# Kernel optimization log

Measured on AMD Instinct MI355X. Metric: run time of the kernel, lower is better.

## Reference

```python
import jax, jax.numpy as jnp
import numpy as np

NUM_HEADS = 12
HEAD_SIZE = 64  # hidden_size // num_heads


def setup_inputs() -> dict:
    key = jax.random.key(0)
    ks = jax.random.split(key, 4)
    B, S, H = 2, 2048, 768
    return {
        "hidden_states": jax.random.normal(ks[0], (B, S, H), dtype=jnp.float32),
        "attention_mask": jnp.ones((B, S), dtype=jnp.int32),
        "Wq": jax.random.normal(ks[1], (H, H), dtype=jnp.float32) * 0.02,
        "bq": jnp.zeros((H,), dtype=jnp.float32),
        "Wk": jax.random.normal(ks[2], (H, H), dtype=jnp.float32) * 0.02,
        "bk": jnp.zeros((H,), dtype=jnp.float32),
        "Wv": jax.random.normal(ks[3], (H, H), dtype=jnp.float32) * 0.02,
        "bv": jnp.zeros((H,), dtype=jnp.float32),
    }


def reference(hidden_states, attention_mask, Wq, bq, Wk, bk, Wv, bv):
    B, S, H = hidden_states.shape
    nh, hs = NUM_HEADS, HEAD_SIZE

    def to_heads(x):  # [B,S,H] -> [nh,B,S,hs] (matches to_multi_head)
        return x.reshape(B, S, nh, hs).transpose(2, 0, 1, 3)

    # torch Linear: y = x @ W.T + b
    q = to_heads(hidden_states @ Wq.T + bq)
    k = to_heads(hidden_states @ Wk.T + bk)
    v = to_heads(hidden_states @ Wv.T + bv)

    scores = jnp.einsum("hbqd,hbkd->hbqk", q, k) / jnp.float32(hs) ** 0.5
    # mask: 1 -> attend, 0 -> -inf; broadcast over query dim
    m = 1.0 - attention_mask.astype(scores.dtype)
    add = jnp.where(m != 0.0, -jnp.inf, 0.0)[None, :, None, :]  # [1,B,1,S]
    probs = jax.nn.softmax(scores + add, axis=-1)
    # dropout is identity in eval mode
    out = jnp.einsum("hbqk,hbkd->hbqd", probs, v)
    # from_multi_head: [nh,B,S,hs] -> [B,S,H]
    return out.transpose(1, 2, 0, 3).reshape(B, S, H)
```

## Files before the change

### kernel.cpp

```cpp
#include <hip/hip_runtime.h>
#include <hip/hip_bf16.h>

#define BATCH 2
#define SEQ   2048
#define HID   768
#define NH    12
#define HS    64
#define MROWS (BATCH*SEQ)
#define N3    (3*HID)
#define HB    (NH*BATCH)

typedef __attribute__((ext_vector_type(8))) short short8;
typedef __attribute__((ext_vector_type(4))) short short4v;
typedef __attribute__((ext_vector_type(4))) float floatx4;

#ifndef __has_builtin
#define __has_builtin(x) 0
#endif
#if __has_builtin(__builtin_amdgcn_mfma_f32_16x16x16bf16_1k)
#define HAVE_K16 1
#else
#define HAVE_K16 0
#endif

#define QSCALE 0.1803368801111204f

__device__ __forceinline__ unsigned short f2bf(float x){
  __hip_bfloat16 h = __float2bfloat16(x);
  return __builtin_bit_cast(unsigned short, h);
}
__device__ __forceinline__ unsigned int f2bf2(float lo, float hi){
  return (unsigned int)f2bf(lo) | ((unsigned int)f2bf(hi) << 16);
}
__device__ __forceinline__ unsigned int f2bf2_rhu(float lo, float hi){
  unsigned int a = __builtin_bit_cast(unsigned int, lo) + 0x8000u;
  unsigned int b = __builtin_bit_cast(unsigned int, hi) + 0x8000u;
  return __builtin_amdgcn_perm(b, a, 0x07060302u);
}
__device__ __forceinline__ float fast_exp2(float x){
  return __builtin_amdgcn_exp2f(x);
}
__device__ __forceinline__ void glds16(const unsigned short* g, unsigned short* l){
  __builtin_amdgcn_global_load_lds(
    (const __attribute__((address_space(1))) unsigned int*)g,
    (__attribute__((address_space(3))) unsigned int*)l, 16, 0, 0);
}

__global__ void f2bf_all_kernel(const float* __restrict__ X,
                                const float* __restrict__ Wq,
                                const float* __restrict__ Wk,
                                const float* __restrict__ Wv,
                                const int* __restrict__ mask,
                                unsigned short* __restrict__ Xb,
                                unsigned short* __restrict__ Wb,
                                float* __restrict__ maskaddG,
                                unsigned int* __restrict__ flagsG){
  const int XQ = MROWS*HID/4;
  const int WQ = HID*HID/4;
  const int NB = (XQ + 3*WQ)/256;
  const int tid = threadIdx.x;
  if(blockIdx.x == NB){
    for(int i=tid;i<BATCH*SEQ;i+=256) maskaddG[i] = mask[i] ? 0.f : -1e30f;
    if(tid < 2) flagsG[tid] = 0u;
    __syncthreads();
    if(tid < BATCH*32){
      int b = tid >> 5, t = tid & 31;
      const int* mrow = mask + b*SEQ + t*64;
      int any = 0;
      for(int i=0;i<64;i++) any |= (mrow[i]==0);
      if(any) atomicOr(&flagsG[b], 1u << t);
    }
    return;
  }
  int i = blockIdx.x * 256 + tid;
  const float* src; unsigned short* dst; int off;
  if(i < XQ){ src = X; dst = Xb; off = i; }
  else {
    int j = i - XQ;
    int w = j / WQ; off = j - w*WQ;
    src = (w==0) ? Wq : (w==1) ? Wk : Wv;
    dst = Wb + (size_t)w*HID*HID;
  }
  float4 v = reinterpret_cast<const float4*>(src)[off];
  ushort4 o;
  o.x = f2bf(v.x); o.y = f2bf(v.y); o.z = f2bf(v.z); o.w = f2bf(v.w);
  reinterpret_cast<ushort4*>(dst)[off] = o;
}

__global__ __launch_bounds__(256) void qkv_gemm_kernel(
    const unsigned short* __restrict__ Xb,
    const unsigned short* __restrict__ Wb,
    const float* __restrict__ bq, const float* __restrict__ bk, const float* __restrict__ bv,
    unsigned short* __restrict__ Qb, unsigned short* __restrict__ Kb,
    unsigned short* __restrict__ Vtb)
{
  __shared__ __align__(16) union {
    struct { unsigned short A[2][128][32]; unsigned short B[2][128][32]; } s;
    unsigned short T[4][64][72];
  } u;
  const int m0 = blockIdx.y << 7;
  const int n0 = blockIdx.x << 7;
  const int tid  = threadIdx.x;
  const int wave = tid >> 6, lane = tid & 63;
  const int wr = wave >> 1, wc = wave & 1;
  const int quad = lane >> 4, l15 = lane & 15;

  const unsigned short* gsrc[4];
  unsigned short* ldst[4];
  #pragma unroll
  for(int p=0;p<4;p++){
    int ck  = ((p&1)<<8) + tid;
    int row = ck>>2, c = ck&3, pc = c ^ (row&3);
    if(p<2){ gsrc[p] = Xb + (size_t)(m0+row)*HID + (pc<<3); ldst[p] = &u.s.A[0][row][c<<3]; }
    else   { gsrc[p] = Wb + (size_t)(n0+row)*HID + (pc<<3); ldst[p] = &u.s.B[0][row][c<<3]; }
  }

  floatx4 acc[4][4];
  #pragma unroll
  for(int i=0;i<4;i++)
    #pragma unroll
    for(int j=0;j<4;j++) acc[i][j] = (floatx4){0.f,0.f,0.f,0.f};

  auto stage = [&](int buf, int k0){
    const int bo = buf*(128*32);
    #pragma unroll
    for(int p=0;p<4;p++) glds16(gsrc[p] + k0, ldst[p] + bo);
  };

  stage(0, 0);
  __syncthreads();

  const int swa = l15 & 3;
  for(int t=0;t<HID/32;t++){
    const int buf = t & 1;
    if(t < HID/32 - 1) stage(buf^1, (t+1)*32);
    short8 a[4], b[4];
    #pragma unroll
    for(int i=0;i<4;i++)
      a[i] = *reinterpret_cast<const short8*>(&u.s.A[buf][wr*64+i*16+l15][(quad^swa)<<3]);
    #pragma unroll
    for(int j=0;j<4;j++)
      b[j] = *reinterpret_cast<const short8*>(&u.s.B[buf][wc*64+j*16+l15][(quad^swa)<<3]);
    #pragma unroll
    for(int i=0;i<4;i++)
      #pragma unroll
      for(int j=0;j<4;j++)
        acc[i][j] = __builtin_amdgcn_mfma_f32_16x16x32_bf16(a[i], b[j], acc[i][j], 0, 0, 0);
    __syncthreads();
  }

  const int which = n0 / HID;
  const int nbase = n0 - which*HID + wc*64;
  const int head  = nbase >> 6;
  const int b_    = m0 >> 11;
  const int hb    = head*BATCH + b_;
  const int s0    = (m0 & 2047) + wr*64;
  if(which < 2){
    unsigned short* dst = which==0 ? Qb : Kb;
    const float* bias = which==0 ? bq : bk;
    const float scale = which==0 ? QSCALE : 1.0f;
    #pragma unroll
    for(int j=0;j<4;j++){
      const float bb = bias[nbase + j*16 + l15];
      #pragma unroll
      for(int i=0;i<4;i++)
        #pragma unroll
        for(int r=0;r<4;r++)
          u.T[wave][i*16 + quad*4 + r][j*16 + l15] = f2bf((acc[i][j][r] + bb)*scale);
    }
    #pragma unroll
    for(int p=0;p<8;p++){
      const int row = p*8 + (lane>>3), dc = (lane&7)*8;
      uint4 v = *reinterpret_cast<const uint4*>(&u.T[wave][row][dc]);
      *reinterpret_cast<uint4*>(dst + ((size_t)(hb<<11) + s0 + row)*HS + dc) = v;
    }
  } else {
    #pragma unroll
    for(int j=0;j<4;j++){
      const float bb = bv[nbase + j*16 + l15];
      #pragma unroll
      for(int i=0;i<4;i++){
        uint2 pk;
        pk.x = f2bf2(acc[i][j][0]+bb, acc[i][j][1]+bb);
        pk.y = f2bf2(acc[i][j][2]+bb, acc[i][j][3]+bb);
        *reinterpret_cast<uint2*>(&u.T[wave][j*16+l15][i*16 + quad*4]) = pk;
      }
    }
    #pragma unroll
    for(int p=0;p<8;p++){
      const int d = p*8 + (lane>>3), cm = lane & 7;
      uint4 v = *reinterpret_cast<const uint4*>(&u.T[wave][d][cm*8]);
      *reinterpret_cast<uint4*>(Vtb + ((size_t)(hb*HS) + d)*SEQ + s0 + cm*8) = v;
    }
  }
}

#if HAVE_K16
__global__ __launch_bounds__(256, 3) void attn_kernel(
    const unsigned short* __restrict__ Qb,
    const unsigned short* __restrict__ Kb,
    const unsigned short* __restrict__ Vtb,
    const float* __restrict__ maskaddG,
    const unsigned int* __restrict__ flagsG,
    float* __restrict__ out)
{
  __shared__ __align__(16) union {
    struct { unsigned short K[2][64][64]; unsigned short V[2][64][64]; } s;
    float Os[64][68];
  } sm;
  __shared__ float lsumS[4][64];

  const int bid = blockIdx.x;
  const int hb = bid >> 5, qt = bid & 31, q0 = qt << 6;
  const int tid = threadIdx.x, wave = tid >> 6, lane = tid & 63;
  const int quad = lane >> 4, l15 = lane & 15;
  const int b_ = hb & 1, head = hb >> 1;

  const unsigned short* gK[2]; const unsigned short* gV[2];
  unsigned short* lK[2]; unsigned short* lV[2];
  #pragma unroll
  for(int p=0;p<2;p++){
    int ck = (p<<8) + tid;
    int row = ck>>3, c = ck&7, pc = c ^ (row&7);
    gK[p] = Kb  + ((size_t)(hb<<11) + row)*HS + (pc<<3);
    lK[p] = &sm.s.K[0][row][c<<3];
    gV[p] = Vtb + ((size_t)(hb*HS) + row)*SEQ + (pc<<3);
    lV[p] = &sm.s.V[0][row][c<<3];
  }
  auto stage = [&](int buf, int k0){
    const int bo = buf*(64*64);
    #pragma unroll
    for(int p=0;p<2;p++){
      glds16(gK[p] + (size_t)k0*HS, lK[p] + bo);
      glds16(gV[p] + k0,           lV[p] + bo);
    }
  };

  stage(0, 0);

  short8 a_q[4][2];
  #pragma unroll
  for(int f=0;f<4;f++){
    const unsigned short* qsrc = Qb + ((size_t)(hb<<11) + q0 + f*16 + l15)*HS;
    a_q[f][0] = *reinterpret_cast<const short8*>(qsrc + quad*8);
    a_q[f][1] = *reinterpret_cast<const short8*>(qsrc + 32 + quad*8);
  }
  const unsigned int fl = flagsG[b_];

  float lsum4[4] = {0.f,0.f,0.f,0.f};
  floatx4 o_acc[4][4];
  #pragma unroll
  for(int f=0;f<4;f++)
    #pragma unroll
    for(int g=0;g<4;g++) o_acc[f][g] = (floatx4){0.f,0.f,0.f,0.f};

  __syncthreads();

  const int sw = l15 & 7;
  const int krow = wave*16 + l15;
  const int vch = ((wave<<1) + (quad>>1)) ^ sw;
  const int voff = (vch<<3) + ((quad&1)<<2);

  for(int t=0;t<SEQ/64;t++){
    const int buf = t & 1, k0 = t << 6;
    if(t < SEQ/64 - 1) stage(buf^1, k0 + 64);

    const unsigned short (*Kst)[64] = sm.s.K[buf];
    const unsigned short (*Vst)[64] = sm.s.V[buf];

    short8 kf0 = *reinterpret_cast<const short8*>(&Kst[krow][(quad^sw)<<3]);
    short8 kf1 = *reinterpret_cast<const short8*>(&Kst[krow][((4+quad)^sw)<<3]);

    floatx4 st[4];
    #pragma unroll
    for(int f=0;f<4;f++) st[f] = (floatx4){0.f,0.f,0.f,0.f};
    #pragma unroll
    for(int f=0;f<4;f++) st[f] = __builtin_amdgcn_mfma_f32_16x16x32_bf16(kf0, a_q[f][0], st[f], 0, 0, 0);
    #pragma unroll
    for(int f=0;f<4;f++) st[f] = __builtin_amdgcn_mfma_f32_16x16x32_bf16(kf1, a_q[f][1], st[f], 0, 0, 0);

    float4 ma = (float4){0.f,0.f,0.f,0.f};
    if((fl >> t) & 1u)
      ma = *reinterpret_cast<const float4*>(maskaddG + (b_<<11) + k0 + wave*16 + quad*4);

    short4v pA[4];
    #pragma unroll
    for(int f=0;f<4;f++){
      float p0 = fast_exp2(st[f][0] + ma.x);
      float p1 = fast_exp2(st[f][1] + ma.y);
      float p2 = fast_exp2(st[f][2] + ma.z);
      float p3 = fast_exp2(st[f][3] + ma.w);
      lsum4[f] += (p0+p1) + (p2+p3);
      union { unsigned int u[2]; short4v s; } pk;
      pk.u[0] = f2bf2_rhu(p0, p1);
      pk.u[1] = f2bf2_rhu(p2, p3);
      pA[f] = pk.s;
    }

    #pragma unroll
    for(int g=0;g<4;g++){
      short4v bvg = *reinterpret_cast<const short4v*>(&Vst[g*16 + l15][voff]);
      #pragma unroll
      for(int f=0;f<4;f++)
        o_acc[f][g] = __builtin_amdgcn_mfma_f32_16x16x16bf16_1k(pA[f], bvg, o_acc[f][g], 0, 0, 0);
    }
    __syncthreads();
  }

  #pragma unroll
  for(int f=0;f<4;f++){
    lsum4[f] += __shfl_xor(lsum4[f], 16);
    lsum4[f] += __shfl_xor(lsum4[f], 32);
  }
  if(lane < 16){
    #pragma unroll
    for(int f=0;f<4;f++) lsumS[wave][f*16 + lane] = lsum4[f];
  }

  #pragma unroll
  for(int w=0;w<4;w++){
    if(wave == w){
      #pragma unroll
      for(int f=0;f<4;f++)
        #pragma unroll
        for(int g=0;g<4;g++){
          floatx4* dst = reinterpret_cast<floatx4*>(&sm.Os[g*16 + l15][f*16 + quad*4]);
          if(w == 0) *dst = o_acc[f][g];
          else      *dst = *dst + o_acc[f][g];
        }
    }
    __syncthreads();
  }

  {
    const int q = tid >> 2, dch = (tid & 3) << 4;
    const float linv = 1.0f /
      (lsumS[0][q] + lsumS[1][q] + lsumS[2][q] + lsumS[3][q]);
    float* orow = out + ((size_t)(b_<<11) + q0 + q)*HID + (head<<6) + dch;
    #pragma unroll
    for(int c4=0;c4<4;c4++){
      float4 o;
      o.x = sm.Os[dch + c4*4 + 0][q] * linv;
      o.y = sm.Os[dch + c4*4 + 1][q] * linv;
      o.z = sm.Os[dch + c4*4 + 2][q] * linv;
      o.w = sm.Os[dch + c4*4 + 3][q] * linv;
      reinterpret_cast<float4*>(orow)[c4] = o;
    }
  }
}
#else
__global__ __launch_bounds__(256) void attn_kernel(
    const unsigned short* __restrict__ Qb,
    const unsigned short* __restrict__ Kb,
    const unsigned short* __restrict__ Vtb,
    const float* __restrict__ maskaddG,
    const unsigned int* __restrict__ flagsG,
    float* __restrict__ out)
{
  __shared__ __align__(16) unsigned short Ks2 [2][64][64];
  __shared__ __align__(16) unsigned short Vts2[2][64][64];
  __shared__ __align__(16) unsigned short Ps2 [4][16][68];

  const int bid = blockIdx.x;
  const int hb = bid >> 5, qt = bid & 31, q0 = qt << 6;
  const int tid = threadIdx.x, wave = tid >> 6, lane = tid & 63;
  const int quad = lane >> 4, l15 = lane & 15;
  const int b_ = hb & 1, head = hb >> 1;

  const unsigned short* gK[2]; const unsigned short* gV[2];
  unsigned short* lK[2]; unsigned short* lV[2];
  #pragma unroll
  for(int p=0;p<2;p++){
    int ck = (p<<8) + tid;
    int row = ck>>3, c = ck&7, pc = c ^ (row&7);
    gK[p] = Kb  + ((size_t)(hb<<11) + row)*HS + (pc<<3);
    lK[p] = &Ks2[0][row][c<<3];
    gV[p] = Vtb + ((size_t)(hb*HS) + row)*SEQ + (pc<<3);
    lV[p] = &Vts2[0][row][c<<3];
  }
  auto stage = [&](int buf, int k0){
    const int bo = buf*(64*64);
    #pragma unroll
    for(int p=0;p<2;p++){
      glds16(gK[p] + (size_t)k0*HS, lK[p] + bo);
      glds16(gV[p] + k0,           lV[p] + bo);
    }
  };

  stage(0, 0);
  short8 a_q[2];
  {
    const unsigned short* qsrc = Qb + ((size_t)(hb<<11) + q0 + wave*16 + l15)*HS;
    a_q[0] = *reinterpret_cast<const short8*>(qsrc + quad*8);
    a_q[1] = *reinterpret_cast<const short8*>(qsrc + 32 + quad*8);
  }
  const unsigned int fl = flagsG[b_];

  float lsum4[4] = {0.f,0.f,0.f,0.f};
  floatx4 o_acc[4];
  #pragma unroll
  for(int dt=0;dt<4;dt++) o_acc[dt] = (floatx4){0.f,0.f,0.f,0.f};

  __syncthreads();

  const int sw = l15 & 7;
  for(int t=0;t<SEQ/64;t++){
    const int buf = t & 1, k0 = t << 6;
    if(t < SEQ/64 - 1) stage(buf^1, k0 + 64);

    const unsigned short (*Kst)[64] = Ks2[buf];
    const unsigned short (*Vst)[64] = Vts2[buf];

    floatx4 st[4];
    #pragma unroll
    for(int kt=0;kt<4;kt++){
      st[kt] = (floatx4){0.f,0.f,0.f,0.f};
      #pragma unroll
      for(int c=0;c<2;c++){
        short8 kf = *reinterpret_cast<const short8*>(
            &Kst[kt*16 + l15][(((c<<2)+quad)^sw)<<3]);
        st[kt] = __builtin_amdgcn_mfma_f32_16x16x32_bf16(kf, a_q[c], st[kt], 0, 0, 0);
      }
    }

    const bool masked = (fl >> t) & 1u;
    #pragma unroll
    for(int kt=0;kt<4;kt++){
      float p0,p1,p2,p3;
      if(!masked){
        p0 = fast_exp2(st[kt][0]); p1 = fast_exp2(st[kt][1]);
        p2 = fast_exp2(st[kt][2]); p3 = fast_exp2(st[kt][3]);
      } else {
        float4 ma = *reinterpret_cast<const float4*>(
            maskaddG + (b_<<11) + k0 + kt*16 + quad*4);
        p0 = fast_exp2(st[kt][0] + ma.x); p1 = fast_exp2(st[kt][1] + ma.y);
        p2 = fast_exp2(st[kt][2] + ma.z); p3 = fast_exp2(st[kt][3] + ma.w);
      }
      lsum4[0] += p0; lsum4[1] += p1; lsum4[2] += p2; lsum4[3] += p3;
      uint2 pk;
      pk.x = f2bf2_rhu(p0, p1);
      pk.y = f2bf2_rhu(p2, p3);
      *reinterpret_cast<uint2*>(&Ps2[wave][l15][kt*16 + quad*4]) = pk;
    }

    short8 ap0, ap1;
    {
      unsigned long long x0 = *reinterpret_cast<const unsigned long long*>(&Ps2[wave][l15][quad*8]);
      unsigned long long x1 = *reinterpret_cast<const unsigned long long*>(&Ps2[wave][l15][quad*8 + 4]);
      unsigned long long y0 = *reinterpret_cast<const unsigned long long*>(&Ps2[wave][l15][32 + quad*8]);
      unsigned long long y1 = *reinterpret_cast<const unsigned long long*>(&Ps2[wave][l15][32 + quad*8 + 4]);
      union { unsigned long long u[2]; short8 s; } cv0, cv1;
      cv0.u[0] = x0; cv0.u[1] = x1;
      cv1.u[0] = y0; cv1.u[1] = y1;
      ap0 = cv0.s; ap1 = cv1.s;
    }
    #pragma unroll
    for(int dt=0;dt<4;dt++){
      short8 bv0 = *reinterpret_cast<const short8*>(&Vst[dt*16 + l15][(quad^sw)<<3]);
      short8 bv1 = *reinterpret_cast<const short8*>(&Vst[dt*16 + l15][((4+quad)^sw)<<3]);
      o_acc[dt] = __builtin_amdgcn_mfma_f32_16x16x32_bf16(ap0, bv0, o_acc[dt], 0, 0, 0);
      o_acc[dt] = __builtin_amdgcn_mfma_f32_16x16x32_bf16(ap1, bv1, o_acc[dt], 0, 0, 0);
    }
    __syncthreads();
  }

  float lsum = (lsum4[0]+lsum4[1]) + (lsum4[2]+lsum4[3]);
  lsum += __shfl_xor(lsum, 16);
  lsum += __shfl_xor(lsum, 32);
  float linv[4];
  #pragma unroll
  for(int r=0;r<4;r++) linv[r] = 1.0f / __shfl(lsum, quad*4 + r);

  #pragma unroll
  for(int dt=0;dt<4;dt++){
    #pragma unroll
    for(int r=0;r<4;r++){
      const int srow = q0 + wave*16 + quad*4 + r;
      out[((size_t)(b_<<11) + srow)*HID + (head<<6) + dt*16 + l15] =
        o_acc[dt][r] * linv[r];
    }
  }
}
#endif

extern "C" void kernel_launch(void* const* d_in, const int* in_sizes, int n_in,
                              void* d_out, int out_size, void* d_ws, size_t ws_size,
                              hipStream_t stream) {
  const float* X    = (const float*)d_in[0];
  const int*   mask = (const int*)  d_in[1];
  const float* Wq   = (const float*)d_in[2];
  const float* bq   = (const float*)d_in[3];
  const float* Wk   = (const float*)d_in[4];
  const float* bk   = (const float*)d_in[5];
  const float* Wv   = (const float*)d_in[6];
  const float* bv   = (const float*)d_in[7];
  float* out = (float*)d_out;

  char* ws = (char*)d_ws;
  unsigned short* Xb  = (unsigned short*)ws;
  unsigned short* Wb  = Xb  + (size_t)MROWS*HID;
  unsigned short* Qb  = Wb  + (size_t)N3*HID;
  unsigned short* Kb  = Qb  + (size_t)HB*SEQ*HS;
  unsigned short* Vtb = Kb  + (size_t)HB*SEQ*HS;
  float* maskaddG = (float*)(Vtb + (size_t)HB*SEQ*HS);
  unsigned int* flagsG = (unsigned int*)(maskaddG + MROWS);

  const int total_quads = (MROWS*HID + 3*HID*HID)/4;
  f2bf_all_kernel<<<total_quads/256 + 1, 256, 0, stream>>>(
      X, Wq, Wk, Wv, mask, Xb, Wb, maskaddG, flagsG);

  qkv_gemm_kernel<<<dim3(N3/128, MROWS/128), 256, 0, stream>>>(
      Xb, Wb, bq, bk, bv, Qb, Kb, Vtb);

  attn_kernel<<<HB*32, 256, 0, stream>>>(
      Qb, Kb, Vtb, maskaddG, flagsG, out);
}
```

Baseline: 160.8 us.

## Fuse fp32-to-bf16 conversion and mask prep into the QKV GEMM

```diff
diff --git a/kernel.cpp b/kernel.cpp
--- a/kernel.cpp
+++ b/kernel.cpp
@@ -46,53 +46,16 @@
     (__attribute__((address_space(3))) unsigned int*)l, 16, 0, 0);
 }
 
-__global__ void f2bf_all_kernel(const float* __restrict__ X,
-                                const float* __restrict__ Wq,
-                                const float* __restrict__ Wk,
-                                const float* __restrict__ Wv,
-                                const int* __restrict__ mask,
-                                unsigned short* __restrict__ Xb,
-                                unsigned short* __restrict__ Wb,
-                                float* __restrict__ maskaddG,
-                                unsigned int* __restrict__ flagsG){
-  const int XQ = MROWS*HID/4;
-  const int WQ = HID*HID/4;
-  const int NB = (XQ + 3*WQ)/256;
-  const int tid = threadIdx.x;
-  if(blockIdx.x == NB){
-    for(int i=tid;i<BATCH*SEQ;i+=256) maskaddG[i] = mask[i] ? 0.f : -1e30f;
-    if(tid < 2) flagsG[tid] = 0u;
-    __syncthreads();
-    if(tid < BATCH*32){
-      int b = tid >> 5, t = tid & 31;
-      const int* mrow = mask + b*SEQ + t*64;
-      int any = 0;
-      for(int i=0;i<64;i++) any |= (mrow[i]==0);
-      if(any) atomicOr(&flagsG[b], 1u << t);
-    }
-    return;
-  }
-  int i = blockIdx.x * 256 + tid;
-  const float* src; unsigned short* dst; int off;
-  if(i < XQ){ src = X; dst = Xb; off = i; }
-  else {
-    int j = i - XQ;
-    int w = j / WQ; off = j - w*WQ;
-    src = (w==0) ? Wq : (w==1) ? Wk : Wv;
-    dst = Wb + (size_t)w*HID*HID;
-  }
-  float4 v = reinterpret_cast<const float4*>(src)[off];
-  ushort4 o;
-  o.x = f2bf(v.x); o.y = f2bf(v.y); o.z = f2bf(v.z); o.w = f2bf(v.w);
-  reinterpret_cast<ushort4*>(dst)[off] = o;
-}
-
 __global__ __launch_bounds__(256) void qkv_gemm_kernel(
-    const unsigned short* __restrict__ Xb,
-    const unsigned short* __restrict__ Wb,
+    const float* __restrict__ X,
+    const float* __restrict__ Wq,
+    const float* __restrict__ Wk,
+    const float* __restrict__ Wv,
+    const int* __restrict__ mask,
     const float* __restrict__ bq, const float* __restrict__ bk, const float* __restrict__ bv,
     unsigned short* __restrict__ Qb, unsigned short* __restrict__ Kb,
-    unsigned short* __restrict__ Vtb)
+    unsigned short* __restrict__ Vtb,
+    float* __restrict__ maskaddG, unsigned int* __restrict__ flagsG)
 {
   __shared__ __align__(16) union {
     struct { unsigned short A[2][128][32]; unsigned short B[2][128][32]; } s;
@@ -104,36 +67,70 @@
   const int wave = tid >> 6, lane = tid & 63;
   const int wr = wave >> 1, wc = wave & 1;
   const int quad = lane >> 4, l15 = lane & 15;
-
-  const unsigned short* gsrc[4];
+  const int which = n0 / HID;
+
+  if(blockIdx.x == 0 && blockIdx.y == 0){
+    for(int i=tid;i<BATCH*SEQ;i+=256) maskaddG[i] = mask[i] ? 0.f : -1e30f;
+    if(tid < 2) flagsG[tid] = 0u;
+    __syncthreads();
+    if(tid < BATCH*32){
+      int b = tid >> 5, t = tid & 31;
+      const int* mrow = mask + b*SEQ + t*64;
+      int any = 0;
+      for(int i=0;i<64;i++) any |= (mrow[i]==0);
+      if(any) atomicOr(&flagsG[b], 1u << t);
+    }
+  }
+
+  const float* gsrcF[4];
   unsigned short* ldst[4];
+  {
+    const float* Wsel = (which==0) ? Wq : (which==1) ? Wk : Wv;
+    const int nloc = n0 - which*HID;
+    #pragma unroll
+    for(int p=0;p<4;p++){
+      int ck  = ((p&1)<<8) + tid;
+      int row = ck>>2, c = ck&3, pc = c ^ (row&3);
+      if(p<2){ gsrcF[p] = X    + (size_t)(m0+row)*HID   + (pc<<3); ldst[p] = &u.s.A[0][row][c<<3]; }
+      else   { gsrcF[p] = Wsel + (size_t)(nloc+row)*HID + (pc<<3); ldst[p] = &u.s.B[0][row][c<<3]; }
+    }
+  }
+
+  floatx4 acc[4][4];
+  #pragma unroll
+  for(int i=0;i<4;i++)
+    #pragma unroll
+    for(int j=0;j<4;j++) acc[i][j] = (floatx4){0.f,0.f,0.f,0.f};
+
+  float4 sreg[4][2];
   #pragma unroll
   for(int p=0;p<4;p++){
-    int ck  = ((p&1)<<8) + tid;
-    int row = ck>>2, c = ck&3, pc = c ^ (row&3);
-    if(p<2){ gsrc[p] = Xb + (size_t)(m0+row)*HID + (pc<<3); ldst[p] = &u.s.A[0][row][c<<3]; }
-    else   { gsrc[p] = Wb + (size_t)(n0+row)*HID + (pc<<3); ldst[p] = &u.s.B[0][row][c<<3]; }
-  }
-
-  floatx4 acc[4][4];
-  #pragma unroll
-  for(int i=0;i<4;i++)
-    #pragma unroll
-    for(int j=0;j<4;j++) acc[i][j] = (floatx4){0.f,0.f,0.f,0.f};
-
-  auto stage = [&](int buf, int k0){
-    const int bo = buf*(128*32);
-    #pragma unroll
-    for(int p=0;p<4;p++) glds16(gsrc[p] + k0, ldst[p] + bo);
-  };
-
-  stage(0, 0);
-  __syncthreads();
+    sreg[p][0] = *reinterpret_cast<const float4*>(gsrcF[p]);
+    sreg[p][1] = *reinterpret_cast<const float4*>(gsrcF[p] + 4);
+  }
 
   const int swa = l15 & 3;
   for(int t=0;t<HID/32;t++){
     const int buf = t & 1;
-    if(t < HID/32 - 1) stage(buf^1, (t+1)*32);
+    const int bo = buf*(128*32);
+    #pragma unroll
+    for(int p=0;p<4;p++){
+      uint4 w;
+      w.x = f2bf2(sreg[p][0].x, sreg[p][0].y);
+      w.y = f2bf2(sreg[p][0].z, sreg[p][0].w);
+      w.z = f2bf2(sreg[p][1].x, sreg[p][1].y);
+      w.w = f2bf2(sreg[p][1].z, sreg[p][1].w);
+      *reinterpret_cast<uint4*>(ldst[p] + bo) = w;
+    }
+    __syncthreads();
+    if(t < HID/32 - 1){
+      const int k0n = (t+1)*32;
+      #pragma unroll
+      for(int p=0;p<4;p++){
+        sreg[p][0] = *reinterpret_cast<const float4*>(gsrcF[p] + k0n);
+        sreg[p][1] = *reinterpret_cast<const float4*>(gsrcF[p] + k0n + 4);
+      }
+    }
     short8 a[4], b[4];
     #pragma unroll
     for(int i=0;i<4;i++)
@@ -149,7 +146,6 @@
     __syncthreads();
   }
 
-  const int which = n0 / HID;
   const int nbase = n0 - which*HID + wc*64;
   const int head  = nbase >> 6;
   const int b_    = m0 >> 11;
@@ -497,20 +493,14 @@
   float* out = (float*)d_out;
 
   char* ws = (char*)d_ws;
-  unsigned short* Xb  = (unsigned short*)ws;
-  unsigned short* Wb  = Xb  + (size_t)MROWS*HID;
-  unsigned short* Qb  = Wb  + (size_t)N3*HID;
-  unsigned short* Kb  = Qb  + (size_t)HB*SEQ*HS;
-  unsigned short* Vtb = Kb  + (size_t)HB*SEQ*HS;
+  unsigned short* Qb  = (unsigned short*)ws;
+  unsigned short* Kb  = Qb + (size_t)HB*SEQ*HS;
+  unsigned short* Vtb = Kb + (size_t)HB*SEQ*HS;
   float* maskaddG = (float*)(Vtb + (size_t)HB*SEQ*HS);
   unsigned int* flagsG = (unsigned int*)(maskaddG + MROWS);
 
-  const int total_quads = (MROWS*HID + 3*HID*HID)/4;
-  f2bf_all_kernel<<<total_quads/256 + 1, 256, 0, stream>>>(
-      X, Wq, Wk, Wv, mask, Xb, Wb, maskaddG, flagsG);
-
   qkv_gemm_kernel<<<dim3(N3/128, MROWS/128), 256, 0, stream>>>(
-      Xb, Wb, bq, bk, bv, Qb, Kb, Vtb);
+      X, Wq, Wk, Wv, mask, bq, bk, bv, Qb, Kb, Vtb, maskaddG, flagsG);
 
   attn_kernel<<<HB*32, 256, 0, stream>>>(
       Qb, Kb, Vtb, maskaddG, flagsG, out);
```

Measured after the change: 165.6 us. 1.03x slower.
